# Kernel optimization log

Measured on AMD Instinct MI355X. Metric: run time of the kernel, lower is better.

Reference implementation:

```python
import math
import jax, jax.numpy as jnp
import numpy as np

BS, N, D, H = 4, 512, 1024, 16
HD = D // H


def setup_inputs() -> dict:
    key = jax.random.key(0)
    ks = jax.random.split(key, 12)
    s = 1.0 / math.sqrt(D)
    return {
        "x": jax.random.normal(ks[0], (BS, N, D), jnp.float32),
        "r": jax.random.normal(ks[1], (BS, 3, N, N), jnp.float32),
        "bias": jax.random.normal(ks[2], (BS, H, N, N), jnp.float32),
        "mask": jax.random.randint(ks[3], (BS, 1, N, N), 0, 2, jnp.int32),
        "wq": jax.random.normal(ks[4], (D, D), jnp.float32) * s,
        "bq": jnp.zeros((D,), jnp.float32),
        "wk": jax.random.normal(ks[5], (D, D), jnp.float32) * s,
        "bk": jnp.zeros((D,), jnp.float32),
        "wv": jax.random.normal(ks[6], (D, D), jnp.float32) * s,
        "bv": jnp.zeros((D,), jnp.float32),
        "wo": jax.random.normal(ks[7], (D, 1), jnp.float32) * s,
        "bo": jnp.zeros((1,), jnp.float32),
    }


def reference(x, r, bias, mask, wq, bq, wk, bk, wv, bv, wo, bo):
    bs, n, d = x.shape
    # projections -> (bs, h, n, hd)
    q = (x @ wq + bq).reshape(bs, n, H, HD).transpose(0, 2, 1, 3)
    k = (x @ wk + bk).reshape(bs, n, H, HD).transpose(0, 2, 1, 3)
    v = (x @ wv + bv).reshape(bs, n, H, HD).transpose(0, 2, 1, 3)
    logits = jnp.einsum("bhid,bhjd->bhij", q, k) / math.sqrt(HD) + bias
    logits = jnp.where(mask == 0, jnp.float32(-1e9), logits)
    w = jax.nn.softmax(logits, axis=-1)  # (bs,h,n,n)
    # o[b,i,c,h,d] = sum_j r[b,c,i,j] * w[b,h,i,j] * v[b,h,j,d]
    o = jnp.einsum("bcij,bhij,bhjd->bichd", r, w, v)
    o = o.reshape(bs, n, 3, d)
    force = o @ wo + bo  # (bs, n, 3, 1)
    return force
```

## Files before the change

### kernel.cpp

```cpp
#include <hip/hip_runtime.h>
#include <hip/hip_fp16.h>
#include <stdint.h>

#define BSZ 4
#define NSEQ 512
#define DMOD 1024
#define NH 16
#define HD 64

typedef __attribute__((ext_vector_type(8))) short bf16x8;
typedef __attribute__((ext_vector_type(4))) float f32x4;

__device__ __forceinline__ unsigned short f2bf(float f) {
    union { float f; uint32_t u; } v; v.f = f;
    uint32_t u = v.u;
    u += 0x7FFFu + ((u >> 16) & 1u);
    return (unsigned short)(u >> 16);
}
__device__ __forceinline__ float bf2f(unsigned short b) {
    union { float f; uint32_t u; } v; v.u = ((uint32_t)b) << 16;
    return v.f;
}

__device__ __forceinline__ void gload_lds16(const unsigned short* g, unsigned short* l) {
    __builtin_amdgcn_global_load_lds(
        (const __attribute__((address_space(1))) void*)g,
        (__attribute__((address_space(3))) void*)l, 16, 0, 0);
}

__global__ __launch_bounds__(256) void k_prep(
        const float* __restrict__ x, const float* __restrict__ wq, const float* __restrict__ wk,
        const float* __restrict__ wv, const float* __restrict__ bv, const float* __restrict__ wo,
        const float* __restrict__ bias, const int* __restrict__ mask,
        unsigned short* __restrict__ xb, unsigned short* __restrict__ wqt,
        unsigned short* __restrict__ wkt, float* __restrict__ wv2t, float* __restrict__ bv2,
        unsigned short* __restrict__ biasm) {
    __shared__ float t[32][33];
    int bx = blockIdx.x, tid = threadIdx.x;
    if (bx < 2048) {
        int i = bx * 256 + tid;
        float4 v = ((const float4*)x)[i];
        ushort4 o; o.x = f2bf(v.x); o.y = f2bf(v.y); o.z = f2bf(v.z); o.w = f2bf(v.w);
        ((ushort4*)xb)[i] = o;
    } else if (bx < 4096) {
        int g = bx - 2048; int z = g >> 10; g &= 1023;
        const float* src = z ? wk : wq;
        unsigned short* dst = z ? wkt : wqt;
        int be = (g & 31) * 32, bc = (g >> 5) * 32;
        int tx = tid & 31, ty = tid >> 5;
        #pragma unroll
        for (int yy = 0; yy < 32; yy += 8)
            t[ty + yy][tx] = src[(size_t)(be + ty + yy) * DMOD + bc + tx];
        __syncthreads();
        #pragma unroll
        for (int yy = 0; yy < 32; yy += 8)
            dst[(size_t)(bc + ty + yy) * DMOD + be + tx] = f2bf(t[tx][ty + yy]);
    } else if (bx < 4352) {
        int g = bx - 4096;
        int grp = tid >> 6, l = tid & 63;
        int e = g * 4 + grp;
        float out = 0.f;
        #pragma unroll
        for (int it = 0; it < 16; ++it) {
            float v = wv[(size_t)e * DMOD + it * 64 + l] * wo[it * 64 + l];
            #pragma unroll
            for (int off = 1; off < 64; off <<= 1) v += __shfl_xor(v, off, 64);
            if (l == it) out = v;
        }
        if (l < 16) wv2t[l * DMOD + e] = out;
        if (g == 0 && grp == 0) {
            float ob = 0.f;
            #pragma unroll
            for (int it = 0; it < 16; ++it) {
                float v = bv[it * 64 + l] * wo[it * 64 + l];
                #pragma unroll
                for (int off = 1; off < 64; off <<= 1) v += __shfl_xor(v, off, 64);
                if (l == it) ob = v;
            }
            if (l < 16) bv2[l] = ob;
        }
    } else {
        int g = bx - 4352;
        int ti = g & 31, h = (g >> 5) & 15, b = g >> 9;
        int l = tid & 63, pb = tid >> 6;
        int quad = l >> 4, col = l & 15;
        const float* brow = bias + (size_t)(b * 16 + h) * NSEQ * NSEQ;
        const int* mrow = mask + (size_t)b * NSEQ * NSEQ;
        #pragma unroll
        for (int pass = 0; pass < 8; ++pass) {
            int tj = pass * 4 + pb;
            int j = tj * 16 + col;
            ushort4 o;
            #pragma unroll
            for (int rr = 0; rr < 4; ++rr) {
                int i = ti * 16 + quad * 4 + rr;
                float bvv = brow[(size_t)i * NSEQ + j];
                int mk = mrow[(size_t)i * NSEQ + j];
                float val = mk ? bvv : -1.0e4f;
                ((unsigned short*)&o)[rr] = __half_as_ushort(__float2half(val));
            }
            size_t tile = ((size_t)((b * 16 + h) * 32 + ti)) * 32 + tj;
            *(ushort4*)(biasm + tile * 256 + l * 4) = o;
        }
    }
}

__global__ __launch_bounds__(256) void k_mid(
        const float* __restrict__ x, const float* __restrict__ wv2t, const float* __restrict__ bv2,
        const unsigned short* __restrict__ xb, const unsigned short* __restrict__ wqt,
        const unsigned short* __restrict__ wkt, const float* __restrict__ bq,
        const float* __restrict__ bk, float* __restrict__ u,
        unsigned short* __restrict__ qT, unsigned short* __restrict__ kT) {
    __shared__ unsigned short lA[64 * 128];
    __shared__ unsigned short lB[64 * 128];
    int bx = blockIdx.x, tid = threadIdx.x;
    if (bx < 512) {
        int wave = bx * 4 + (tid >> 6);
        int l = tid & 63;
        int b = wave >> 9, j = wave & 511;
        const float* xr = x + (size_t)(b * NSEQ + j) * DMOD;
        float p[16];
        #pragma unroll
        for (int h = 0; h < 16; ++h) p[h] = 0.f;
        for (int it = 0; it < 16; ++it) {
            int e = l + it * 64;
            float xv = xr[e];
            #pragma unroll
            for (int h = 0; h < 16; ++h) p[h] += xv * wv2t[h * DMOD + e];
        }
        #pragma unroll
        for (int h = 0; h < 16; ++h) {
            #pragma unroll
            for (int off = 1; off < 64; off <<= 1) p[h] += __shfl_xor(p[h], off, 64);
        }
        float out = 0.f;
        #pragma unroll
        for (int h = 0; h < 16; ++h) if (l == h) out = p[h] + bv2[h];
        if (l < 16) u[(b * 16 + l) * NSEQ + j] = out;
        return;
    }
    int g = bx - 512;
    int z = g >> 9;
    const unsigned short* Wt = z ? wkt : wqt;
    const float* bias = z ? bk : bq;
    unsigned short* outT = z ? kT : qT;
    float scale = z ? 1.f : 0.125f;
    int w = tid >> 6, lane = tid & 63;
    int quad = lane >> 4, col = lane & 15;
    int m0 = (g & 31) * 64;
    int n0 = ((g >> 5) & 15) * 64;

    f32x4 acc[4];
    #pragma unroll
    for (int nt = 0; nt < 4; ++nt) acc[nt] = (f32x4){0.f, 0.f, 0.f, 0.f};

    int rl_base = lane >> 4;
    int cs = lane & 15;
    int asw = cs & 7;

    for (int kc = 0; kc < 8; ++kc) {
        int k0 = kc * 128;
        #pragma unroll
        for (int t = 0; t < 4; ++t) {
            int rl = t * 4 + rl_base;
            int row = w * 16 + rl;
            int cg = cs ^ (rl & 7);
            gload_lds16(xb + (size_t)(m0 + row) * DMOD + k0 + cg * 8,
                        &lA[(w * 16 + t * 4) * 128]);
            gload_lds16(Wt + (size_t)(n0 + row) * DMOD + k0 + cg * 8,
                        &lB[(w * 16 + t * 4) * 128]);
        }
        __syncthreads();
        int arow = w * 16 + cs;
        #pragma unroll
        for (int ks = 0; ks < 4; ++ks) {
            int blk = (ks * 4 + quad) ^ asw;
            bf16x8 af = *(const bf16x8*)&lA[arow * 128 + blk * 8];
            #pragma unroll
            for (int nt = 0; nt < 4; ++nt) {
                bf16x8 bfr = *(const bf16x8*)&lB[(nt * 16 + cs) * 128 + blk * 8];
                acc[nt] = __builtin_amdgcn_mfma_f32_16x16x32_bf16(af, bfr, acc[nt], 0, 0, 0);
            }
        }
        __syncthreads();
    }
    #pragma unroll
    for (int nt = 0; nt < 4; ++nt) {
        int n = n0 + nt * 16 + col;
        int h = n >> 6, d = n & 63;
        float bvv = bias[n];
        #pragma unroll
        for (int r = 0; r < 4; ++r) {
            int mg = m0 + w * 16 + quad * 4 + r;
            int b = mg >> 9, i = mg & 511;
            outT[(size_t)((b * 16 + h) * NSEQ + i) * HD + d] = f2bf((acc[nt][r] + bvv) * scale);
        }
    }
}

__global__ __launch_bounds__(256) void k_logits(
        const unsigned short* __restrict__ qT, const unsigned short* __restrict__ kT,
        const unsigned short* __restrict__ biasm,
        unsigned short* __restrict__ eW, float* __restrict__ spart) {
    __shared__ unsigned short elds[4][16][66];
    int tid = threadIdx.x, w = tid >> 6, lane = tid & 63;
    int quad = lane >> 4, col = lane & 15;
    int bx = blockIdx.x;
    int it = bx & 7, jc = (bx >> 3) & 7, h = (bx >> 6) & 15, b = bx >> 10;
    int bh = b * 16 + h;
    int i0 = it * 64 + w * 16;
    int j0 = jc * 64;

    const unsigned short* qbase = qT + ((size_t)(bh * NSEQ + i0 + col)) * HD + quad * 8;
    bf16x8 a0 = *(const bf16x8*)qbase;
    bf16x8 a1 = *(const bf16x8*)(qbase + 32);

    bf16x8 kf0[4], kf1[4];
    uint2 bm[4];
    #pragma unroll
    for (int jt = 0; jt < 4; ++jt) {
        const unsigned short* kbase = kT + ((size_t)(bh * NSEQ + j0 + jt * 16 + col)) * HD + quad * 8;
        kf0[jt] = *(const bf16x8*)kbase;
        kf1[jt] = *(const bf16x8*)(kbase + 32);
        size_t tile = ((size_t)(bh * 32 + it * 4 + w)) * 32 + (jc * 4 + jt);
        bm[jt] = *(const uint2*)(biasm + tile * 256 + lane * 4);
    }

    float sp[4] = {0.f, 0.f, 0.f, 0.f};
    #pragma unroll
    for (int jt = 0; jt < 4; ++jt) {
        f32x4 acc = (f32x4){0.f, 0.f, 0.f, 0.f};
        acc = __builtin_amdgcn_mfma_f32_16x16x32_bf16(a0, kf0[jt], acc, 0, 0, 0);
        acc = __builtin_amdgcn_mfma_f32_16x16x32_bf16(a1, kf1[jt], acc, 0, 0, 0);
        unsigned short hb[4];
        hb[0] = (unsigned short)(bm[jt].x & 0xffffu);
        hb[1] = (unsigned short)(bm[jt].x >> 16);
        hb[2] = (unsigned short)(bm[jt].y & 0xffffu);
        hb[3] = (unsigned short)(bm[jt].y >> 16);
        #pragma unroll
        for (int rr = 0; rr < 4; ++rr) {
            float lg = acc[rr] + __half2float(__ushort_as_half(hb[rr]));
            float ev = __expf(lg);
            sp[rr] += ev;
            elds[w][quad * 4 + rr][jt * 16 + col] = f2bf(ev);
        }
    }
    #pragma unroll
    for (int rr = 0; rr < 4; ++rr) {
        #pragma unroll
        for (int off = 1; off < 16; off <<= 1) sp[rr] += __shfl_xor(sp[rr], off, 64);
    }
    if (col == 0) {
        #pragma unroll
        for (int rr = 0; rr < 4; ++rr)
            spart[((size_t)(bh * NSEQ) + i0 + quad * 4 + rr) * 8 + jc] = sp[rr];
    }
    __syncthreads();
    #pragma unroll
    for (int k2 = 0; k2 < 8; ++k2) {
        int row = (lane >> 5) + k2 * 2;
        int jseg = (lane & 31) * 2;
        uint32_t val = *(const uint32_t*)&elds[w][row][jseg];
        int i = i0 + row;
        *(uint32_t*)(eW + (((size_t)(b * NSEQ + i) * NH + h) * NSEQ) + j0 + jseg) = val;
    }
}

__global__ __launch_bounds__(256) void k_combine(
        const unsigned short* __restrict__ eW, const float* __restrict__ spart,
        const float* __restrict__ u, const float* __restrict__ r,
        const float* __restrict__ bo, float* __restrict__ out) {
    __shared__ __align__(16) unsigned short elds[2][NH][NSEQ];
    __shared__ float su[2][16];
    __shared__ float red[2][2][3];
    int tid = threadIdx.x, bx = blockIdx.x;
    int ip = bx & 255, b = bx >> 8;
    int i0 = ip * 2;
    const unsigned short* esrc = eW + (size_t)(b * NSEQ + i0) * NH * NSEQ;
    #pragma unroll
    for (int t = 0; t < 8; ++t)
        ((int4*)&elds[0][0][0])[tid + t * 256] = ((const int4*)esrc)[tid + t * 256];
    {
        int il = tid >> 7, hq = (tid >> 3) & 15, jcq = tid & 7;
        float v = spart[((size_t)((b * 16 + hq) * NSEQ) + i0 + il) * 8 + jcq];
        v += __shfl_xor(v, 1, 64); v += __shfl_xor(v, 2, 64); v += __shfl_xor(v, 4, 64);
        if (jcq == 0) su[il][hq] = (v > 0.f) ? 1.f / v : 0.f;
    }
    __syncthreads();
    int il = tid >> 7, jj = tid & 127, j = jj * 4;
    int i = i0 + il;
    float s0 = 0.f, s1 = 0.f, s2 = 0.f, s3 = 0.f;
    #pragma unroll
    for (int h = 0; h < 16; ++h) {
        float wgt = su[il][h];
        float4 uv = *(const float4*)(u + (size_t)(b * 16 + h) * NSEQ + j);
        uint2 ep = *(const uint2*)&elds[il][h][j];
        s0 += bf2f((unsigned short)(ep.x & 0xffffu)) * wgt * uv.x;
        s1 += bf2f((unsigned short)(ep.x >> 16)) * wgt * uv.y;
        s2 += bf2f((unsigned short)(ep.y & 0xffffu)) * wgt * uv.z;
        s3 += bf2f((unsigned short)(ep.y >> 16)) * wgt * uv.w;
    }
    float acc[3];
    #pragma unroll
    for (int c = 0; c < 3; ++c) {
        float4 rv = *(const float4*)(r + ((size_t)(b * 3 + c) * NSEQ + i) * NSEQ + j);
        acc[c] = rv.x * s0 + rv.y * s1 + rv.z * s2 + rv.w * s3;
    }
    #pragma unroll
    for (int c = 0; c < 3; ++c) {
        #pragma unroll
        for (int off = 1; off < 64; off <<= 1) acc[c] += __shfl_xor(acc[c], off, 64);
    }
    int wv = tid >> 6, lane = tid & 63;
    if (lane == 0) {
        red[wv >> 1][wv & 1][0] = acc[0];
        red[wv >> 1][wv & 1][1] = acc[1];
        red[wv >> 1][wv & 1][2] = acc[2];
    }
    __syncthreads();
    if (tid < 6) {
        int ilo = tid / 3, c = tid % 3;
        out[(size_t)(b * NSEQ + i0 + ilo) * 3 + c] = red[ilo][0][c] + red[ilo][1][c] + bo[0];
    }
}

extern "C" void kernel_launch(void* const* d_in, const int* in_sizes, int n_in,
                              void* d_out, int out_size, void* d_ws, size_t ws_size,
                              hipStream_t stream) {
    const float* x    = (const float*)d_in[0];
    const float* rr   = (const float*)d_in[1];
    const float* bias = (const float*)d_in[2];
    const int*   mask = (const int*)d_in[3];
    const float* wq   = (const float*)d_in[4];
    const float* bq   = (const float*)d_in[5];
    const float* wk   = (const float*)d_in[6];
    const float* bk   = (const float*)d_in[7];
    const float* wv   = (const float*)d_in[8];
    const float* bv   = (const float*)d_in[9];
    const float* wo   = (const float*)d_in[10];
    const float* bo   = (const float*)d_in[11];
    float* out = (float*)d_out;

    char* ws = (char*)d_ws;
    unsigned short* xb   = (unsigned short*)(ws + 0);
    unsigned short* wqt  = (unsigned short*)(ws + 4194304);
    unsigned short* wkt  = (unsigned short*)(ws + 6291456);
    float*          wv2t = (float*)(ws + 8388608);
    float*          bv2  = (float*)(ws + 8454144);
    float*          u    = (float*)(ws + 8454400);
    unsigned short* qT   = (unsigned short*)(ws + 8585472);
    unsigned short* kT   = (unsigned short*)(ws + 12779776);
    unsigned short* bm   = (unsigned short*)(ws + 16974080);
    unsigned short* eW   = (unsigned short*)(ws + 50528512);
    float*          spart= (float*)(ws + 84082944);

    k_prep<<<6400, 256, 0, stream>>>(x, wq, wk, wv, bv, wo, bias, mask,
                                     xb, wqt, wkt, wv2t, bv2, bm);
    k_mid<<<1536, 256, 0, stream>>>(x, wv2t, bv2, xb, wqt, wkt, bq, bk, u, qT, kT);
    k_logits<<<4096, 256, 0, stream>>>(qT, kT, bm, eW, spart);
    k_combine<<<1024, 256, 0, stream>>>(eW, spart, u, rr, bo, out);
}
```

Before: 208.1 us.

## Fuse bias/mask read and r-weighted combine into attention kernel

```diff
diff --git a/kernel.cpp b/kernel.cpp
--- a/kernel.cpp
+++ b/kernel.cpp
@@ -1,5 +1,4 @@
 #include <hip/hip_runtime.h>
-#include <hip/hip_fp16.h>
 #include <stdint.h>
 
 #define BSZ 4
@@ -17,10 +16,6 @@
     u += 0x7FFFu + ((u >> 16) & 1u);
     return (unsigned short)(u >> 16);
 }
-__device__ __forceinline__ float bf2f(unsigned short b) {
-    union { float f; uint32_t u; } v; v.u = ((uint32_t)b) << 16;
-    return v.f;
-}
 
 __device__ __forceinline__ void gload_lds16(const unsigned short* g, unsigned short* l) {
     __builtin_amdgcn_global_load_lds(
@@ -31,10 +26,8 @@
 __global__ __launch_bounds__(256) void k_prep(
         const float* __restrict__ x, const float* __restrict__ wq, const float* __restrict__ wk,
         const float* __restrict__ wv, const float* __restrict__ bv, const float* __restrict__ wo,
-        const float* __restrict__ bias, const int* __restrict__ mask,
         unsigned short* __restrict__ xb, unsigned short* __restrict__ wqt,
-        unsigned short* __restrict__ wkt, float* __restrict__ wv2t, float* __restrict__ bv2,
-        unsigned short* __restrict__ biasm) {
+        unsigned short* __restrict__ wkt, float* __restrict__ wv2t, float* __restrict__ bv2) {
     __shared__ float t[32][33];
     int bx = blockIdx.x, tid = threadIdx.x;
     if (bx < 2048) {
@@ -55,7 +48,7 @@
         #pragma unroll
         for (int yy = 0; yy < 32; yy += 8)
             dst[(size_t)(bc + ty + yy) * DMOD + be + tx] = f2bf(t[tx][ty + yy]);
-    } else if (bx < 4352) {
+    } else {
         int g = bx - 4096;
         int grp = tid >> 6, l = tid & 63;
         int e = g * 4 + grp;
@@ -78,29 +71,6 @@
                 if (l == it) ob = v;
             }
             if (l < 16) bv2[l] = ob;
-        }
-    } else {
-        int g = bx - 4352;
-        int ti = g & 31, h = (g >> 5) & 15, b = g >> 9;
-        int l = tid & 63, pb = tid >> 6;
-        int quad = l >> 4, col = l & 15;
-        const float* brow = bias + (size_t)(b * 16 + h) * NSEQ * NSEQ;
-        const int* mrow = mask + (size_t)b * NSEQ * NSEQ;
-        #pragma unroll
-        for (int pass = 0; pass < 8; ++pass) {
-            int tj = pass * 4 + pb;
-            int j = tj * 16 + col;
-            ushort4 o;
-            #pragma unroll
-            for (int rr = 0; rr < 4; ++rr) {
-                int i = ti * 16 + quad * 4 + rr;
-                float bvv = brow[(size_t)i * NSEQ + j];
-                int mk = mrow[(size_t)i * NSEQ + j];
-                float val = mk ? bvv : -1.0e4f;
-                ((unsigned short*)&o)[rr] = __half_as_ushort(__float2half(val));
-            }
-            size_t tile = ((size_t)((b * 16 + h) * 32 + ti)) * 32 + tj;
-            *(ushort4*)(biasm + tile * 256 + l * 4) = o;
         }
     }
 }
@@ -198,129 +168,125 @@
     }
 }
 
-__global__ __launch_bounds__(256) void k_logits(
+#define RSTRIDE 68
+__global__ __launch_bounds__(512) void k_attn(
         const unsigned short* __restrict__ qT, const unsigned short* __restrict__ kT,
-        const unsigned short* __restrict__ biasm,
-        unsigned short* __restrict__ eW, float* __restrict__ spart) {
-    __shared__ unsigned short elds[4][16][66];
-    int tid = threadIdx.x, w = tid >> 6, lane = tid & 63;
+        const float* __restrict__ bias, const int* __restrict__ mask,
+        const float* __restrict__ u, const float* __restrict__ r,
+        float* __restrict__ spart, float* __restrict__ P) {
+    __shared__ float rT[3 * 16 * RSTRIDE];
+    int tid = threadIdx.x;
+    int w = tid >> 6, lane = tid & 63;
     int quad = lane >> 4, col = lane & 15;
-    int bx = blockIdx.x;
-    int it = bx & 7, jc = (bx >> 3) & 7, h = (bx >> 6) & 15, b = bx >> 10;
+    int it = blockIdx.x, jc = blockIdx.y, b = blockIdx.z;
+    int i0 = it * 16, j0 = jc * 64;
+
+    #pragma unroll
+    for (int t = 0; t < 6; ++t) {
+        int idx = t * 512 + tid;
+        int c = idx >> 10, rem = idx & 1023;
+        int i = rem >> 6, j = rem & 63;
+        rT[(c * 16 + i) * RSTRIDE + j] =
+            r[((size_t)(b * 3 + c) * NSEQ + i0 + i) * NSEQ + j0 + j];
+    }
+    const int* mrow = mask + (size_t)b * NSEQ * NSEQ;
+    __syncthreads();
+
+    #pragma unroll
+    for (int hrep = 0; hrep < 2; ++hrep) {
+        int h = w + hrep * 8;
+        int bh = b * 16 + h;
+        const unsigned short* qbase = qT + ((size_t)(bh * NSEQ + i0 + col)) * HD + quad * 8;
+        bf16x8 a0 = *(const bf16x8*)qbase;
+        bf16x8 a1 = *(const bf16x8*)(qbase + 32);
+        const float* brow = bias + (size_t)bh * NSEQ * NSEQ;
+        const float* ub = u + (size_t)bh * NSEQ;
+        float sp[4] = {0.f, 0.f, 0.f, 0.f};
+        float pc0[4] = {0.f, 0.f, 0.f, 0.f};
+        float pc1[4] = {0.f, 0.f, 0.f, 0.f};
+        float pc2[4] = {0.f, 0.f, 0.f, 0.f};
+        #pragma unroll
+        for (int jt = 0; jt < 4; ++jt) {
+            int jb = j0 + jt * 16;
+            const unsigned short* kbase = kT + ((size_t)(bh * NSEQ + jb + col)) * HD + quad * 8;
+            bf16x8 b0 = *(const bf16x8*)kbase;
+            bf16x8 b1 = *(const bf16x8*)(kbase + 32);
+            f32x4 acc = (f32x4){0.f, 0.f, 0.f, 0.f};
+            acc = __builtin_amdgcn_mfma_f32_16x16x32_bf16(a0, b0, acc, 0, 0, 0);
+            acc = __builtin_amdgcn_mfma_f32_16x16x32_bf16(a1, b1, acc, 0, 0, 0);
+            int j = jb + col;
+            float uv = ub[j];
+            int jl = jt * 16 + col;
+            #pragma unroll
+            for (int rr = 0; rr < 4; ++rr) {
+                int i = i0 + quad * 4 + rr;
+                float lg = acc[rr] + brow[(size_t)i * NSEQ + j];
+                int mk = mrow[(size_t)i * NSEQ + j];
+                float e = (mk == 0) ? 0.f : __expf(lg);
+                sp[rr] += e;
+                float eu = e * uv;
+                int il = quad * 4 + rr;
+                pc0[rr] += eu * rT[(0 * 16 + il) * RSTRIDE + jl];
+                pc1[rr] += eu * rT[(1 * 16 + il) * RSTRIDE + jl];
+                pc2[rr] += eu * rT[(2 * 16 + il) * RSTRIDE + jl];
+            }
+        }
+        #pragma unroll
+        for (int rr = 0; rr < 4; ++rr) {
+            #pragma unroll
+            for (int off = 1; off < 16; off <<= 1) {
+                sp[rr]  += __shfl_xor(sp[rr], off, 64);
+                pc0[rr] += __shfl_xor(pc0[rr], off, 64);
+                pc1[rr] += __shfl_xor(pc1[rr], off, 64);
+                pc2[rr] += __shfl_xor(pc2[rr], off, 64);
+            }
+        }
+        if (col == 0) {
+            #pragma unroll
+            for (int rr = 0; rr < 4; ++rr) {
+                int il = quad * 4 + rr;
+                spart[((size_t)bh * NSEQ + i0 + il) * 8 + jc] = sp[rr];
+                size_t pb = ((((size_t)(b * 16 + h) * 32 + it) * 8 + jc) * 16 + il) * 3;
+                P[pb + 0] = pc0[rr];
+                P[pb + 1] = pc1[rr];
+                P[pb + 2] = pc2[rr];
+            }
+        }
+    }
+}
+
+__global__ __launch_bounds__(256) void k_final(
+        const float* __restrict__ spart, const float* __restrict__ P,
+        const float* __restrict__ bo, float* __restrict__ out) {
+    int tid = threadIdx.x;
+    int rloc = tid >> 4, h = tid & 15;
+    int row = blockIdx.x * 16 + rloc;
+    int b = row >> 9, i = row & 511;
+    int it = i >> 4, il = i & 15;
     int bh = b * 16 + h;
-    int i0 = it * 64 + w * 16;
-    int j0 = jc * 64;
-
-    const unsigned short* qbase = qT + ((size_t)(bh * NSEQ + i0 + col)) * HD + quad * 8;
-    bf16x8 a0 = *(const bf16x8*)qbase;
-    bf16x8 a1 = *(const bf16x8*)(qbase + 32);
-
-    bf16x8 kf0[4], kf1[4];
-    uint2 bm[4];
-    #pragma unroll
-    for (int jt = 0; jt < 4; ++jt) {
-        const unsigned short* kbase = kT + ((size_t)(bh * NSEQ + j0 + jt * 16 + col)) * HD + quad * 8;
-        kf0[jt] = *(const bf16x8*)kbase;
-        kf1[jt] = *(const bf16x8*)(kbase + 32);
-        size_t tile = ((size_t)(bh * 32 + it * 4 + w)) * 32 + (jc * 4 + jt);
-        bm[jt] = *(const uint2*)(biasm + tile * 256 + lane * 4);
-    }
-
-    float sp[4] = {0.f, 0.f, 0.f, 0.f};
-    #pragma unroll
-    for (int jt = 0; jt < 4; ++jt) {
-        f32x4 acc = (f32x4){0.f, 0.f, 0.f, 0.f};
-        acc = __builtin_amdgcn_mfma_f32_16x16x32_bf16(a0, kf0[jt], acc, 0, 0, 0);
-        acc = __builtin_amdgcn_mfma_f32_16x16x32_bf16(a1, kf1[jt], acc, 0, 0, 0);
-        unsigned short hb[4];
-        hb[0] = (unsigned short)(bm[jt].x & 0xffffu);
-        hb[1] = (unsigned short)(bm[jt].x >> 16);
-        hb[2] = (unsigned short)(bm[jt].y & 0xffffu);
-        hb[3] = (unsigned short)(bm[jt].y >> 16);
-        #pragma unroll
-        for (int rr = 0; rr < 4; ++rr) {
-            float lg = acc[rr] + __half2float(__ushort_as_half(hb[rr]));
-            float ev = __expf(lg);
-            sp[rr] += ev;
-            elds[w][quad * 4 + rr][jt * 16 + col] = f2bf(ev);
-        }
-    }
-    #pragma unroll
-    for (int rr = 0; rr < 4; ++rr) {
-        #pragma unroll
-        for (int off = 1; off < 16; off <<= 1) sp[rr] += __shfl_xor(sp[rr], off, 64);
-    }
-    if (col == 0) {
-        #pragma unroll
-        for (int rr = 0; rr < 4; ++rr)
-            spart[((size_t)(bh * NSEQ) + i0 + quad * 4 + rr) * 8 + jc] = sp[rr];
-    }
-    __syncthreads();
-    #pragma unroll
-    for (int k2 = 0; k2 < 8; ++k2) {
-        int row = (lane >> 5) + k2 * 2;
-        int jseg = (lane & 31) * 2;
-        uint32_t val = *(const uint32_t*)&elds[w][row][jseg];
-        int i = i0 + row;
-        *(uint32_t*)(eW + (((size_t)(b * NSEQ + i) * NH + h) * NSEQ) + j0 + jseg) = val;
-    }
-}
-
-__global__ __launch_bounds__(256) void k_combine(
-        const unsigned short* __restrict__ eW, const float* __restrict__ spart,
-        const float* __restrict__ u, const float* __restrict__ r,
-        const float* __restrict__ bo, float* __restrict__ out) {
-    __shared__ __align__(16) unsigned short elds[2][NH][NSEQ];
-    __shared__ float su[2][16];
-    __shared__ float red[2][2][3];
-    int tid = threadIdx.x, bx = blockIdx.x;
-    int ip = bx & 255, b = bx >> 8;
-    int i0 = ip * 2;
-    const unsigned short* esrc = eW + (size_t)(b * NSEQ + i0) * NH * NSEQ;
-    #pragma unroll
-    for (int t = 0; t < 8; ++t)
-        ((int4*)&elds[0][0][0])[tid + t * 256] = ((const int4*)esrc)[tid + t * 256];
-    {
-        int il = tid >> 7, hq = (tid >> 3) & 15, jcq = tid & 7;
-        float v = spart[((size_t)((b * 16 + hq) * NSEQ) + i0 + il) * 8 + jcq];
-        v += __shfl_xor(v, 1, 64); v += __shfl_xor(v, 2, 64); v += __shfl_xor(v, 4, 64);
-        if (jcq == 0) su[il][hq] = (v > 0.f) ? 1.f / v : 0.f;
-    }
-    __syncthreads();
-    int il = tid >> 7, jj = tid & 127, j = jj * 4;
-    int i = i0 + il;
-    float s0 = 0.f, s1 = 0.f, s2 = 0.f, s3 = 0.f;
-    #pragma unroll
-    for (int h = 0; h < 16; ++h) {
-        float wgt = su[il][h];
-        float4 uv = *(const float4*)(u + (size_t)(b * 16 + h) * NSEQ + j);
-        uint2 ep = *(const uint2*)&elds[il][h][j];
-        s0 += bf2f((unsigned short)(ep.x & 0xffffu)) * wgt * uv.x;
-        s1 += bf2f((unsigned short)(ep.x >> 16)) * wgt * uv.y;
-        s2 += bf2f((unsigned short)(ep.y & 0xffffu)) * wgt * uv.z;
-        s3 += bf2f((unsigned short)(ep.y >> 16)) * wgt * uv.w;
-    }
-    float acc[3];
-    #pragma unroll
-    for (int c = 0; c < 3; ++c) {
-        float4 rv = *(const float4*)(r + ((size_t)(b * 3 + c) * NSEQ + i) * NSEQ + j);
-        acc[c] = rv.x * s0 + rv.y * s1 + rv.z * s2 + rv.w * s3;
-    }
-    #pragma unroll
-    for (int c = 0; c < 3; ++c) {
-        #pragma unroll
-        for (int off = 1; off < 64; off <<= 1) acc[c] += __shfl_xor(acc[c], off, 64);
-    }
-    int wv = tid >> 6, lane = tid & 63;
-    if (lane == 0) {
-        red[wv >> 1][wv & 1][0] = acc[0];
-        red[wv >> 1][wv & 1][1] = acc[1];
-        red[wv >> 1][wv & 1][2] = acc[2];
-    }
-    __syncthreads();
-    if (tid < 6) {
-        int ilo = tid / 3, c = tid % 3;
-        out[(size_t)(b * NSEQ + i0 + ilo) * 3 + c] = red[ilo][0][c] + red[ilo][1][c] + bo[0];
+    const float* sprow = spart + ((size_t)bh * NSEQ + i) * 8;
+    float4 sa = *(const float4*)sprow;
+    float4 sb = *(const float4*)(sprow + 4);
+    float s = sa.x + sa.y + sa.z + sa.w + sb.x + sb.y + sb.z + sb.w;
+    float sinv = (s > 0.f) ? 1.f / s : 0.f;
+    float f0 = 0.f, f1 = 0.f, f2 = 0.f;
+    #pragma unroll
+    for (int jc = 0; jc < 8; ++jc) {
+        size_t pb = ((((size_t)(b * 16 + h) * 32 + it) * 8 + jc) * 16 + il) * 3;
+        f0 += P[pb]; f1 += P[pb + 1]; f2 += P[pb + 2];
+    }
+    f0 *= sinv; f1 *= sinv; f2 *= sinv;
+    #pragma unroll
+    for (int off = 1; off < 16; off <<= 1) {
+        f0 += __shfl_xor(f0, off, 64);
+        f1 += __shfl_xor(f1, off, 64);
+        f2 += __shfl_xor(f2, off, 64);
+    }
+    if (h == 0) {
+        float bov = bo[0];
+        out[(size_t)row * 3 + 0] = f0 + bov;
+        out[(size_t)row * 3 + 1] = f1 + bov;
+        out[(size_t)row * 3 + 2] = f2 + bov;
     }
 }
 
@@ -342,21 +308,19 @@
     float* out = (float*)d_out;
 
     char* ws = (char*)d_ws;
-    unsigned short* xb   = (unsigned short*)(ws + 0);
-    unsigned short* wqt  = (unsigned short*)(ws + 4194304);
-    unsigned short* wkt  = (unsigned short*)(ws + 6291456);
-    float*          wv2t = (float*)(ws + 8388608);
-    float*          bv2  = (float*)(ws + 8454144);
-    float*          u    = (float*)(ws + 8454400);
-    unsigned short* qT   = (unsigned short*)(ws + 8585472);
-    unsigned short* kT   = (unsigned short*)(ws + 12779776);
-    unsigned short* bm   = (unsigned short*)(ws + 16974080);
-    unsigned short* eW   = (unsigned short*)(ws + 50528512);
-    float*          spart= (float*)(ws + 84082944);
-
-    k_prep<<<6400, 256, 0, stream>>>(x, wq, wk, wv, bv, wo, bias, mask,
-                                     xb, wqt, wkt, wv2t, bv2, bm);
+    unsigned short* xb    = (unsigned short*)(ws + 0);
+    unsigned short* wqt   = (unsigned short*)(ws + 4194304);
+    unsigned short* wkt   = (unsigned short*)(ws + 6291456);
+    float*          wv2t  = (float*)(ws + 8388608);
+    float*          bv2   = (float*)(ws + 8454144);
+    float*          u     = (float*)(ws + 8454400);
+    unsigned short* qT    = (unsigned short*)(ws + 8585472);
+    unsigned short* kT    = (unsigned short*)(ws + 12779776);
+    float*          spart = (float*)(ws + 16974080);
+    float*          P     = (float*)(ws + 18022656);
+
+    k_prep<<<4352, 256, 0, stream>>>(x, wq, wk, wv, bv, wo, xb, wqt, wkt, wv2t, bv2);
     k_mid<<<1536, 256, 0, stream>>>(x, wv2t, bv2, xb, wqt, wkt, bq, bk, u, qT, kT);
-    k_logits<<<4096, 256, 0, stream>>>(qT, kT, bm, eW, spart);
-    k_combine<<<1024, 256, 0, stream>>>(eW, spart, u, rr, bo, out);
-}
+    k_attn<<<dim3(32, 8, 4), 512, 0, stream>>>(qT, kT, bias, mask, u, rr, spart, P);
+    k_final<<<128, 256, 0, stream>>>(spart, P, bo, out);
+}
```

Measured after the change: 223.0 us. 1.07x slower.
